# Kernel tuning notes

Measured on AMD Instinct MI355X. Metric: run time of the kernel, lower is better.

The kernel has to match this reference:

```python
import jax, jax.numpy as jnp
import numpy as np

MAX_DEG = 10   # max_degree in DuvenaudMPNN
T = 4          # num_timesteps
NUM_GRAPHS = 64


def setup_inputs() -> dict:
    key = jax.random.key(0)
    ks = jax.random.split(key, 10)
    N, E, IN, EC = 20000, 160000, 64, 16
    s = 0.1
    x = jax.random.normal(ks[0], (N, IN), dtype=jnp.float32)
    edge_index = jax.random.randint(ks[1], (2, E), 0, N)
    edge_attr = jax.random.normal(ks[2], (E, EC), dtype=jnp.float32)
    batch = jnp.sort(jax.random.randint(ks[3], (N,), 0, NUM_GRAPHS))
    # per-timestep, per-degree expert Linear(in+e -> in, bias=False)
    W_msg = jax.random.normal(ks[4], (T, MAX_DEG, IN + EC, IN), dtype=jnp.float32) * s
    # per-timestep readout Linear(in -> 10, bias=False)
    W_read = jax.random.normal(ks[5], (T, IN, 10), dtype=jnp.float32) * s
    fc1_w = jax.random.normal(ks[6], (10, 128), dtype=jnp.float32) * s
    fc1_b = jnp.zeros((128,), jnp.float32)
    fc2_w = jax.random.normal(ks[7], (128, 64), dtype=jnp.float32) * s
    fc2_b = jnp.zeros((64,), jnp.float32)
    fc3_w = jax.random.normal(ks[8], (64, 1), dtype=jnp.float32) * s
    fc3_b = jnp.zeros((1,), jnp.float32)
    return {"x": x, "edge_attr": edge_attr, "W_msg": W_msg, "W_read": W_read,
            "fc1_w": fc1_w, "fc1_b": fc1_b, "fc2_w": fc2_w, "fc2_b": fc2_b,
            "fc3_w": fc3_w, "fc3_b": fc3_b, "edge_index": edge_index, "batch": batch}


def _mpnn(x, edge_attr, W_msg, W_read, edge_index):
    N = x.shape[0]
    # add_self_loops: append (i,i) edges with zero edge features
    self_idx = jnp.arange(N, dtype=edge_index.dtype)
    src = jnp.concatenate([edge_index[0], self_idx])
    dst = jnp.concatenate([edge_index[1], self_idx])
    ea = jnp.concatenate([edge_attr, jnp.zeros((N, edge_attr.shape[1]), edge_attr.dtype)], axis=0)
    # degree of source node (incl. self loop), clamped to MAX_DEG; bucket 0..MAX_DEG-1
    deg = jax.ops.segment_sum(jnp.ones_like(src), src, num_segments=N)
    bucket = jnp.minimum(deg[src], MAX_DEG) - 1
    Etot = src.shape[0]
    for t in range(T):
        mi = jnp.concatenate([x[src], ea], axis=-1)           # [Etot, IN+EC]
        msgs = jnp.zeros((Etot, x.shape[1]), x.dtype)
        for d in range(MAX_DEG):                               # degree-bucketed experts
            md = jax.nn.sigmoid(mi @ W_msg[t, d])              # [Etot, IN]
            msgs = jnp.where((bucket == d)[:, None], md, msgs)
        x = jax.ops.segment_sum(msgs, dst, num_segments=N)    # aggr='add'
    # readout: all timestep heads applied to final x, softmax over outputs, summed
    node_out = jax.nn.softmax(x @ W_read[0], axis=1)
    for t in range(1, T):
        node_out = node_out + jax.nn.softmax(x @ W_read[t], axis=1)
    return node_out                                            # [N, 10]


def reference(x, edge_attr, W_msg, W_read, fc1_w, fc1_b, fc2_w, fc2_b, fc3_w, fc3_b, edge_index, batch):
    node_out = _mpnn(x, edge_attr, W_msg, W_read, edge_index)
    pooled = jax.ops.segment_sum(node_out, batch, num_segments=NUM_GRAPHS)  # global_add_pool
    h = jax.nn.leaky_relu(pooled @ fc1_w + fc1_b)
    h = jax.nn.leaky_relu(h @ fc2_w + fc2_b)
    return jax.nn.leaky_relu(h @ fc3_w + fc3_b)                # [NUM_GRAPHS, 1]
```

## Files before the change

### kernel.cpp

```cpp
#include <hip/hip_runtime.h>

#define MAXD 10
#define TSTEPS 4
#define KD 80
#define IN 64
#define ECH 16
#define TILE_N 64
#define SCAN_CHUNK 1024

#define AGG_BLOCK 256
#define AGG_DPB (AGG_BLOCK / 16)

__device__ __forceinline__ float sigmoidf(float v) {
    return 1.0f / (1.0f + __expf(-v));
}


__global__ __launch_bounds__(256) void hist_kernel(const int* __restrict__ ei,
                                                   int* deg, int* in_cnt, int E) {
    int e = blockIdx.x * 256 + threadIdx.x;
    if (e < E) {
        atomicAdd(&deg[ei[e]], 1);
        atomicAdd(&in_cnt[ei[E + e]], 1);
    }
}


__global__ __launch_bounds__(256) void scanA_kernel(const int* __restrict__ in_cnt,
                                                    const int* __restrict__ deg,
                                                    int* bsum, int* nb_cnt, int N) {
    __shared__ int part[256];
    __shared__ int nbh[MAXD];
    const int t = threadIdx.x;
    if (t < MAXD) nbh[t] = 0;
    __syncthreads();
    const int base = blockIdx.x * SCAN_CHUNK + t * 4;
    int s = 0;
    #pragma unroll
    for (int i = 0; i < 4; ++i) {
        int gi = base + i;
        if (gi < N) {
            s += in_cnt[gi];
            int dg = deg[gi];
            int b = (dg < MAXD - 1) ? dg : (MAXD - 1);
            atomicAdd(&nbh[b], 1);
        }
    }
    part[t] = s;
    __syncthreads();
    for (int off = 128; off > 0; off >>= 1) {
        if (t < off) part[t] += part[t + off];
        __syncthreads();
    }
    if (t == 0) bsum[blockIdx.x] = part[0];
    if (t < MAXD && nbh[t] > 0) atomicAdd(&nb_cnt[t], nbh[t]);
}

__global__ __launch_bounds__(256) void scanB_kernel(int* bsum, int nb,
                                                    const int* __restrict__ nb_cnt,
                                                    int* nb_cursor, int* row_ptr,
                                                    int N, int E) {
    __shared__ int part[256];
    const int t = threadIdx.x;
    int v = (t < nb) ? bsum[t] : 0;
    part[t] = v;
    __syncthreads();
    for (int off = 1; off < 256; off <<= 1) {
        int add = (t >= off) ? part[t - off] : 0;
        __syncthreads();
        part[t] += add;
        __syncthreads();
    }
    if (t < nb) bsum[t] = part[t] - v;
    if (t == 0) {
        int acc = 0;
        for (int b = 0; b < MAXD; ++b) { nb_cursor[b] = acc; acc += nb_cnt[b]; }
        row_ptr[N] = E;
    }
}

__global__ __launch_bounds__(256) void scanC_kernel(const int* __restrict__ in_cnt,
                                                    const int* __restrict__ bsum,
                                                    int* cursorN, int* row_ptr, int N) {
    __shared__ int part[256];
    const int t = threadIdx.x;
    const int base = blockIdx.x * SCAN_CHUNK + t * 4;
    int v[4] = {0, 0, 0, 0};
    #pragma unroll
    for (int i = 0; i < 4; ++i) if (base + i < N) v[i] = in_cnt[base + i];
    const int s = v[0] + v[1] + v[2] + v[3];
    part[t] = s;
    __syncthreads();
    for (int off = 1; off < 256; off <<= 1) {
        int add = (t >= off) ? part[t - off] : 0;
        __syncthreads();
        part[t] += add;
        __syncthreads();
    }
    int a = bsum[blockIdx.x] + part[t] - s;
    #pragma unroll
    for (int i = 0; i < 4; ++i) {
        if (base + i < N) { cursorN[base + i] = a; row_ptr[base + i] = a; }
        a += v[i];
    }
}

__global__ __launch_bounds__(256) void nb_scatter_kernel(const int* __restrict__ deg,
                                                         int* cursor, int* node_list, int N) {
    __shared__ int h[MAXD];
    __shared__ int base[MAXD];
    const int t = threadIdx.x;
    if (t < MAXD) h[t] = 0;
    __syncthreads();
    const int n = blockIdx.x * 256 + t;
    int b = 0, loc = 0;
    const bool valid = n < N;
    if (valid) {
        int dg = deg[n];
        b = (dg < MAXD - 1) ? dg : (MAXD - 1);
        loc = atomicAdd(&h[b], 1);
    }
    __syncthreads();
    if (t < MAXD) base[t] = (h[t] > 0) ? atomicAdd(&cursor[t], h[t]) : 0;
    __syncthreads();
    if (valid) node_list[base[b] + loc] = n;
}

__global__ __launch_bounds__(256) void csr_scatter_kernel(
    const int* __restrict__ ei, const float* __restrict__ ea, const int* __restrict__ deg,
    int* cursor, int* src_csr, int* bkt_csr, float* ea_csr, int E)
{
    int e = blockIdx.x * 256 + threadIdx.x;
    if (e >= E) return;
    int s = ei[e], d = ei[E + e];
    int dg = deg[s];
    int b = (dg < MAXD - 1) ? dg : (MAXD - 1);
    int pos = atomicAdd(&cursor[d], 1);
    src_csr[pos] = s;
    bkt_csr[pos] = b;
    const float4* p = (const float4*)(ea + (size_t)e * ECH);
    float4* o = (float4*)(ea_csr + (size_t)pos * ECH);
    o[0] = p[0]; o[1] = p[1]; o[2] = p[2]; o[3] = p[3];
}


__global__ __launch_bounds__(256) void y_kernel(
    const float* __restrict__ xin, float* __restrict__ y,
    const int* __restrict__ node_list, const int* __restrict__ deg,
    const float* __restrict__ Wt, int N)
{
    __shared__ float Ws[IN][IN];
    __shared__ float Ms[IN][TILE_N + 4];
    __shared__ int id_s[TILE_N];
    __shared__ int bkt_s[TILE_N];

    const int t = threadIdx.x;
    const int i0 = blockIdx.x * TILE_N;
    const int ntile = min(TILE_N, N - i0);

    {
        const int e = t >> 2;
        const bool valid = e < ntile;
        const int c0 = (t & 3) * 16;
        const float4 z4 = make_float4(0.f, 0.f, 0.f, 0.f);
        int node = valid ? node_list[i0 + e] : 0;
        const float* xp = xin + (size_t)node * IN + c0;
        #pragma unroll
        for (int i = 0; i < 16; i += 4) {
            float4 v = valid ? *(const float4*)(xp + i) : z4;
            Ms[c0 + i + 0][e] = v.x; Ms[c0 + i + 1][e] = v.y;
            Ms[c0 + i + 2][e] = v.z; Ms[c0 + i + 3][e] = v.w;
        }
        if (t < TILE_N) {
            if (t < ntile) {
                int id = node_list[i0 + t];
                id_s[t] = id;
                int dg = deg[id];
                bkt_s[t] = (dg < MAXD - 1) ? dg : (MAXD - 1);
            } else { id_s[t] = 0; bkt_s[t] = -1; }
        }
    }
    __syncthreads();

    const int b_first = bkt_s[0];
    const int b_last = bkt_s[ntile - 1];
    const int eg4 = (t >> 4) * 4;
    const int cg4 = (t & 15) * 4;

    for (int b = b_first; b <= b_last; ++b) {
        if (b != b_first) __syncthreads();
        {
            const float4* Wb = (const float4*)(Wt + (size_t)b * KD * IN);
            float4* Wsp = (float4*)Ws;
            #pragma unroll
            for (int q = 0; q < 4; ++q) Wsp[t + q * 256] = Wb[t + q * 256];
        }
        __syncthreads();

        float acc[4][4];
        #pragma unroll
        for (int e2 = 0; e2 < 4; ++e2)
            #pragma unroll
            for (int c = 0; c < 4; ++c) acc[e2][c] = 0.f;

        #pragma unroll 8
        for (int k = 0; k < IN; ++k) {
            const float4 w = *(const float4*)&Ws[k][cg4];
            const float4 m = *(const float4*)&Ms[k][eg4];
            const float me[4] = {m.x, m.y, m.z, m.w};
            #pragma unroll
            for (int e2 = 0; e2 < 4; ++e2) {
                acc[e2][0] += me[e2] * w.x;
                acc[e2][1] += me[e2] * w.y;
                acc[e2][2] += me[e2] * w.z;
                acc[e2][3] += me[e2] * w.w;
            }
        }

        #pragma unroll
        for (int e2 = 0; e2 < 4; ++e2) {
            const int el = eg4 + e2;
            if (el < ntile && bkt_s[el] == b) {
                const size_t o = (size_t)id_s[el] * IN + cg4;
                *(float4*)(y + o) = make_float4(acc[e2][0], acc[e2][1],
                                                acc[e2][2], acc[e2][3]);
            }
        }
    }
}


__global__ __launch_bounds__(AGG_BLOCK) void agg6_kernel(
    const float* __restrict__ y, float* __restrict__ out,
    const int* __restrict__ row_ptr, const int* __restrict__ src_csr,
    const int* __restrict__ bkt_csr, const float* __restrict__ ea_csr,
    const float* __restrict__ Wt, int N)
{
    __shared__ float WeL[MAXD][ECH][IN];
    const int t = threadIdx.x;
    {
        const float4* Wsrc = (const float4*)Wt;
        float4* Wd = (float4*)WeL;
        #pragma unroll
        for (int i = 0; i < MAXD * ECH * IN / 4 / AGG_BLOCK; ++i) {
            int q = t + i * AGG_BLOCK;
            int b = q >> 8;
            int r = q & 255;
            Wd[q] = Wsrc[b * (KD * IN / 4) + (IN * IN / 4) + r];
        }
    }
    __syncthreads();

    const int lane = t & 63;
    const int grp = lane >> 4;
    const int gl = lane & 15;
    const int c0 = gl * 4;
    const int d = blockIdx.x * AGG_DPB + (t >> 6) * 4 + grp;
    if (d >= N) return;
    const int lane0 = grp * 16;

    const int p0 = row_ptr[d];
    const int p1 = row_ptr[d + 1];

    float4 acc = make_float4(0.f, 0.f, 0.f, 0.f);

    for (int p = p0; p < p1; p += 8) {
        const int cnt = min(8, p1 - p);
        const int mi = p + (gl & 7);
        int s_r = 0, b_r = 0;
        if (mi < p1) { s_r = src_csr[mi]; b_r = bkt_csr[mi]; }

        float4 yv[8];
        #pragma unroll
        for (int i = 0; i < 8; ++i) {
            int si = __shfl(s_r, lane0 + i);
            if (i < cnt) yv[i] = *(const float4*)(y + (size_t)si * IN + c0);
        }

        const float4* eab = (const float4*)(ea_csr + (size_t)p * ECH);
        float4 ca0 = eab[0], ca1 = eab[1], ca2 = eab[2], ca3 = eab[3];

        #pragma unroll
        for (int i = 0; i < 8; ++i) {
            if (i < cnt) {
                float4 na0, na1, na2, na3;
                if (i + 1 < cnt) {
                    const float4* ep = (const float4*)(ea_csr + (size_t)(p + i + 1) * ECH);
                    na0 = ep[0]; na1 = ep[1]; na2 = ep[2]; na3 = ep[3];
                } else {
                    na0 = na1 = na2 = na3 = make_float4(0.f, 0.f, 0.f, 0.f);
                }
                const int b = __shfl(b_r, lane0 + i);
                const float ev[16] = {ca0.x, ca0.y, ca0.z, ca0.w, ca1.x, ca1.y, ca1.z, ca1.w,
                                      ca2.x, ca2.y, ca2.z, ca2.w, ca3.x, ca3.y, ca3.z, ca3.w};
                float4 z = make_float4(0.f, 0.f, 0.f, 0.f);
                #pragma unroll
                for (int k = 0; k < ECH; ++k) {
                    const float4 w = *(const float4*)&WeL[b][k][c0];
                    z.x += ev[k] * w.x; z.y += ev[k] * w.y;
                    z.z += ev[k] * w.z; z.w += ev[k] * w.w;
                }
                acc.x += sigmoidf(yv[i].x + z.x);
                acc.y += sigmoidf(yv[i].y + z.y);
                acc.z += sigmoidf(yv[i].z + z.z);
                acc.w += sigmoidf(yv[i].w + z.w);
                ca0 = na0; ca1 = na1; ca2 = na2; ca3 = na3;
            }
        }
    }

    const float4 yd = *(const float4*)(y + (size_t)d * IN + c0);
    float4 r = make_float4(sigmoidf(yd.x) + acc.x, sigmoidf(yd.y) + acc.y,
                           sigmoidf(yd.z) + acc.z, sigmoidf(yd.w) + acc.w);
    *(float4*)(out + (size_t)d * IN + c0) = r;
}


__global__ __launch_bounds__(256) void readout_kernel(
    const float* __restrict__ x, const float* __restrict__ Wr,
    const int* __restrict__ batch, float* __restrict__ pooled, int N)
{
    __shared__ float Wr_s[TSTEPS][10][IN];
    __shared__ float pool_s[64 * 10];
    const int t = threadIdx.x;
    for (int idx = t; idx < TSTEPS * IN * 10; idx += 256) {
        int tt = idx / (IN * 10);
        int r = idx % (IN * 10);
        int k = r / 10;
        int j = r % 10;
        Wr_s[tt][j][k] = Wr[idx];
    }
    for (int idx = t; idx < 64 * 10; idx += 256) pool_s[idx] = 0.f;
    __syncthreads();

    const int n = blockIdx.x * 256 + t;
    if (n < N) {
        float xr[IN];
        const float4* xp = (const float4*)(x + (size_t)n * IN);
        #pragma unroll
        for (int i = 0; i < IN / 4; ++i) ((float4*)xr)[i] = xp[i];
        float out10[10];
        #pragma unroll
        for (int j = 0; j < 10; ++j) out10[j] = 0.f;
        for (int tt = 0; tt < TSTEPS; ++tt) {
            float lg[10];
            #pragma unroll
            for (int j = 0; j < 10; ++j) {
                const float4* wp = (const float4*)Wr_s[tt][j];
                float s = 0.f;
                #pragma unroll
                for (int i = 0; i < IN / 4; ++i) {
                    float4 w = wp[i];
                    float4 xv = ((const float4*)xr)[i];
                    s += w.x * xv.x + w.y * xv.y + w.z * xv.z + w.w * xv.w;
                }
                lg[j] = s;
            }
            float mx = lg[0];
            #pragma unroll
            for (int j = 1; j < 10; ++j) mx = fmaxf(mx, lg[j]);
            float sum = 0.f;
            #pragma unroll
            for (int j = 0; j < 10; ++j) { lg[j] = __expf(lg[j] - mx); sum += lg[j]; }
            float inv = 1.f / sum;
            #pragma unroll
            for (int j = 0; j < 10; ++j) out10[j] += lg[j] * inv;
        }
        const int g = batch[n];
        #pragma unroll
        for (int j = 0; j < 10; ++j) atomicAdd(&pool_s[g * 10 + j], out10[j]);
    }
    __syncthreads();
    for (int idx = t; idx < 64 * 10; idx += 256) {
        float v = pool_s[idx];
        if (v != 0.f) atomicAdd(&pooled[idx], v);
    }
}


__global__ __launch_bounds__(256) void mlp_kernel(
    const float* __restrict__ pooled,
    const float* __restrict__ fc1w, const float* __restrict__ fc1b,
    const float* __restrict__ fc2w, const float* __restrict__ fc2b,
    const float* __restrict__ fc3w, const float* __restrict__ fc3b,
    float* __restrict__ out, int G)
{
    __shared__ float p_s[64 * 10];
    __shared__ float h1[64 * 128];
    __shared__ float h2[64 * 64];
    const int t = threadIdx.x;
    for (int idx = t; idx < G * 10; idx += 256) p_s[idx] = pooled[idx];
    __syncthreads();
    for (int idx = t; idx < G * 128; idx += 256) {
        int g = idx >> 7, j = idx & 127;
        float s = fc1b[j];
        #pragma unroll
        for (int k = 0; k < 10; ++k) s += p_s[g * 10 + k] * fc1w[k * 128 + j];
        h1[idx] = (s > 0.f) ? s : 0.01f * s;
    }
    __syncthreads();
    for (int idx = t; idx < G * 64; idx += 256) {
        int g = idx >> 6, j = idx & 63;
        float s = fc2b[j];
        for (int k = 0; k < 128; ++k) s += h1[(g << 7) + k] * fc2w[(k << 6) + j];
        h2[idx] = (s > 0.f) ? s : 0.01f * s;
    }
    __syncthreads();
    if (t < G) {
        float s = fc3b[0];
        for (int k = 0; k < 64; ++k) s += h2[(t << 6) + k] * fc3w[k];
        out[t] = (s > 0.f) ? s : 0.01f * s;
    }
}


extern "C" void kernel_launch(void* const* d_in, const int* in_sizes, int n_in,
                              void* d_out, int out_size, void* d_ws, size_t ws_size,
                              hipStream_t stream)
{
    const float* x     = (const float*)d_in[0];
    const float* ea    = (const float*)d_in[1];
    const float* Wmsg  = (const float*)d_in[2];
    const float* Wread = (const float*)d_in[3];
    const float* fc1w  = (const float*)d_in[4];
    const float* fc1b  = (const float*)d_in[5];
    const float* fc2w  = (const float*)d_in[6];
    const float* fc2b  = (const float*)d_in[7];
    const float* fc3w  = (const float*)d_in[8];
    const float* fc3b  = (const float*)d_in[9];
    const int* ei      = (const int*)d_in[10];
    const int* batch   = (const int*)d_in[11];

    const int N = in_sizes[0] / IN;
    const int E = in_sizes[10] / 2;
    const int nscan = (N + SCAN_CHUNK - 1) / SCAN_CHUNK;

    char* ws = (char*)d_ws;
    size_t off = 0;
    auto take = [&](size_t bytes) {
        char* p = ws + off;
        off = (off + bytes + 255) & ~(size_t)255;
        return p;
    };
    int* meta      = (int*)take(128);
    float* pooled  = (float*)take(64 * 10 * 4);
    int* deg       = (int*)take((size_t)N * 4);
    int* in_cnt    = (int*)take((size_t)N * 4);
    const size_t zero_bytes = (size_t)((char*)in_cnt - (char*)meta) + (size_t)N * 4;
    int* bsum      = (int*)take((size_t)nscan * 4);
    int* node_list = (int*)take((size_t)N * 4);
    int* cursorN   = (int*)take((size_t)N * 4);
    int* row_ptr   = (int*)take((size_t)(N + 1) * 4);
    int* src_csr   = (int*)take((size_t)E * 4);
    int* bkt_csr   = (int*)take((size_t)E * 4);
    float* ea_csr  = (float*)take((size_t)E * ECH * 4);
    float* ybuf    = (float*)take((size_t)N * IN * 4);
    float* xbA     = (float*)take((size_t)N * IN * 4);
    float* xbB     = (float*)take((size_t)N * IN * 4);

    int* nb_cnt    = meta;
    int* nb_cursor = meta + 16;

    const int nbN = (N + 255) / 256;
    const int nbE = (E + 255) / 256;

    hipMemsetAsync(meta, 0, zero_bytes, stream);
    hist_kernel<<<nbE, 256, 0, stream>>>(ei, deg, in_cnt, E);
    scanA_kernel<<<nscan, 256, 0, stream>>>(in_cnt, deg, bsum, nb_cnt, N);
    scanB_kernel<<<1, 256, 0, stream>>>(bsum, nscan, nb_cnt, nb_cursor, row_ptr, N, E);
    scanC_kernel<<<nscan, 256, 0, stream>>>(in_cnt, bsum, cursorN, row_ptr, N);
    nb_scatter_kernel<<<nbN, 256, 0, stream>>>(deg, nb_cursor, node_list, N);
    csr_scatter_kernel<<<nbE, 256, 0, stream>>>(ei, ea, deg, cursorN,
                                                src_csr, bkt_csr, ea_csr, E);

    const int nblkY = (N + TILE_N - 1) / TILE_N;
    const int nblkA = (N + AGG_DPB - 1) / AGG_DPB;
    const float* xi = x;
    float* bufs[2] = {xbA, xbB};
    for (int tt = 0; tt < TSTEPS; ++tt) {
        const float* Wt = Wmsg + (size_t)tt * MAXD * KD * IN;
        float* xo = bufs[tt & 1];
        y_kernel<<<nblkY, 256, 0, stream>>>(xi, ybuf, node_list, deg, Wt, N);
        agg6_kernel<<<nblkA, AGG_BLOCK, 0, stream>>>(ybuf, xo, row_ptr, src_csr,
                                                     bkt_csr, ea_csr, Wt, N);
        xi = xo;
    }

    readout_kernel<<<nbN, 256, 0, stream>>>(xi, Wread, batch, pooled, N);
    mlp_kernel<<<1, 256, 0, stream>>>(pooled, fc1w, fc1b, fc2w, fc2b, fc3w, fc3b,
                                      (float*)d_out, out_size);
}
```

Baseline: 310.7 us.

## Precompute edge-feature message terms for all timesteps in bucket-sorted batched GEMM

Edges are now also scattered into degree-bucket order, and one batched kernel computes the edge-attribute projection ea·W_e for every timestep up front into a [T,E,64] buffer. The per-timestep aggregation kernel then only gathers the precomputed z rows through a CSR-to-bucket index instead of doing a 16-deep per-edge matvec from shared-memory weights. This removes the per-edge FMA work and the 40KB shared-memory weight load from the aggregation kernel. In exchange it writes and reads about 164MB of extra z data, so the gather becomes more memory-bound.

New measurement: 304.2 us. -2.1%, faster.

```diff
diff --git a/kernel.cpp b/kernel.cpp
--- a/kernel.cpp
+++ b/kernel.cpp
@@ -6,6 +6,7 @@
 #define IN 64
 #define ECH 16
 #define TILE_N 64
+#define TILE_Z 128
 #define SCAN_CHUNK 1024
 
 #define AGG_BLOCK 256
@@ -25,14 +26,15 @@
     }
 }
 
-
 __global__ __launch_bounds__(256) void scanA_kernel(const int* __restrict__ in_cnt,
                                                     const int* __restrict__ deg,
-                                                    int* bsum, int* nb_cnt, int N) {
+                                                    int* bsum, int* nb_cnt, int* eb_cnt,
+                                                    int N) {
     __shared__ int part[256];
     __shared__ int nbh[MAXD];
-    const int t = threadIdx.x;
-    if (t < MAXD) nbh[t] = 0;
+    __shared__ int ebh[MAXD];
+    const int t = threadIdx.x;
+    if (t < MAXD) { nbh[t] = 0; ebh[t] = 0; }
     __syncthreads();
     const int base = blockIdx.x * SCAN_CHUNK + t * 4;
     int s = 0;
@@ -44,6 +46,7 @@
             int dg = deg[gi];
             int b = (dg < MAXD - 1) ? dg : (MAXD - 1);
             atomicAdd(&nbh[b], 1);
+            if (dg > 0) atomicAdd(&ebh[b], dg);
         }
     }
     part[t] = s;
@@ -53,13 +56,18 @@
         __syncthreads();
     }
     if (t == 0) bsum[blockIdx.x] = part[0];
-    if (t < MAXD && nbh[t] > 0) atomicAdd(&nb_cnt[t], nbh[t]);
+    if (t < MAXD) {
+        if (nbh[t] > 0) atomicAdd(&nb_cnt[t], nbh[t]);
+        if (ebh[t] > 0) atomicAdd(&eb_cnt[t], ebh[t]);
+    }
 }
 
 __global__ __launch_bounds__(256) void scanB_kernel(int* bsum, int nb,
                                                     const int* __restrict__ nb_cnt,
-                                                    int* nb_cursor, int* row_ptr,
-                                                    int N, int E) {
+                                                    int* nb_cursor,
+                                                    const int* __restrict__ eb_cnt,
+                                                    int* eb_cursor, int* eb_base,
+                                                    int* row_ptr, int N, int E) {
     __shared__ int part[256];
     const int t = threadIdx.x;
     int v = (t < nb) ? bsum[t] : 0;
@@ -75,6 +83,11 @@
     if (t == 0) {
         int acc = 0;
         for (int b = 0; b < MAXD; ++b) { nb_cursor[b] = acc; acc += nb_cnt[b]; }
+        acc = 0;
+        for (int b = 0; b < MAXD; ++b) {
+            eb_cursor[b] = acc; eb_base[b] = acc; acc += eb_cnt[b];
+        }
+        eb_base[MAXD] = E;
         row_ptr[N] = E;
     }
 }
@@ -126,21 +139,119 @@
     if (valid) node_list[base[b] + loc] = n;
 }
 
-__global__ __launch_bounds__(256) void csr_scatter_kernel(
+__global__ __launch_bounds__(256) void edge_scatter_kernel(
     const int* __restrict__ ei, const float* __restrict__ ea, const int* __restrict__ deg,
-    int* cursor, int* src_csr, int* bkt_csr, float* ea_csr, int E)
-{
-    int e = blockIdx.x * 256 + threadIdx.x;
-    if (e >= E) return;
-    int s = ei[e], d = ei[E + e];
-    int dg = deg[s];
-    int b = (dg < MAXD - 1) ? dg : (MAXD - 1);
-    int pos = atomicAdd(&cursor[d], 1);
-    src_csr[pos] = s;
-    bkt_csr[pos] = b;
-    const float4* p = (const float4*)(ea + (size_t)e * ECH);
-    float4* o = (float4*)(ea_csr + (size_t)pos * ECH);
-    o[0] = p[0]; o[1] = p[1]; o[2] = p[2]; o[3] = p[3];
+    int* cursorN, int* eb_cursor,
+    int* src_csr, int* csr2bkt, float* ea_bkt, int E)
+{
+    __shared__ int h[MAXD];
+    __shared__ int hbase[MAXD];
+    const int t = threadIdx.x;
+    if (t < MAXD) h[t] = 0;
+    __syncthreads();
+    const int e = blockIdx.x * 256 + t;
+    const bool valid = e < E;
+    int s = 0, d = 0, b = 0, loc = 0;
+    if (valid) {
+        s = ei[e]; d = ei[E + e];
+        int dg = deg[s];
+        b = (dg < MAXD - 1) ? dg : (MAXD - 1);
+        loc = atomicAdd(&h[b], 1);
+    }
+    __syncthreads();
+    if (t < MAXD) hbase[t] = (h[t] > 0) ? atomicAdd(&eb_cursor[t], h[t]) : 0;
+    __syncthreads();
+    if (valid) {
+        const int posz = hbase[b] + loc;
+        const int pos = atomicAdd(&cursorN[d], 1);
+        src_csr[pos] = s;
+        csr2bkt[pos] = posz;
+        const float4* p = (const float4*)(ea + (size_t)e * ECH);
+        float4* o = (float4*)(ea_bkt + (size_t)posz * ECH);
+        o[0] = p[0]; o[1] = p[1]; o[2] = p[2]; o[3] = p[3];
+    }
+}
+
+
+__global__ __launch_bounds__(256) void zgemm_kernel(
+    const float* __restrict__ ea_bkt, float* __restrict__ zs,
+    const int* __restrict__ eb_base, const float* __restrict__ Wmsg,
+    int E, int ntiles)
+{
+    __shared__ float Ez[ECH][TILE_Z + 4];
+    __shared__ int ebase_s[MAXD + 1];
+
+    const int t = threadIdx.x;
+    const int bid = blockIdx.x;
+    const int tt = bid / ntiles;
+    const int i0 = (bid % ntiles) * TILE_Z;
+    const float* Wt = Wmsg + (size_t)tt * MAXD * KD * IN;
+    float* zt = zs + (size_t)tt * E * IN;
+    const int ntile = min(TILE_Z, E - i0);
+
+    if (t <= MAXD) ebase_s[t] = eb_base[t];
+    {
+        const int e = t >> 1;
+        const int j0 = (t & 1) * 8;
+        const bool valid = e < ntile;
+        const float4 z4 = make_float4(0.f, 0.f, 0.f, 0.f);
+        const float* ep = ea_bkt + (size_t)(i0 + e) * ECH + j0;
+        #pragma unroll
+        for (int i = 0; i < 8; i += 4) {
+            float4 v = valid ? *(const float4*)(ep + i) : z4;
+            Ez[j0 + i + 0][e] = v.x; Ez[j0 + i + 1][e] = v.y;
+            Ez[j0 + i + 2][e] = v.z; Ez[j0 + i + 3][e] = v.w;
+        }
+    }
+    __syncthreads();
+
+    const int eg8 = (t >> 4) * 8;
+    const int cg4 = (t & 15) * 4;
+
+    int b = 0;
+    #pragma unroll
+    for (int q = 1; q < MAXD; ++q) if (ebase_s[q] <= i0) b = q;
+
+    for (; b < MAXD; ++b) {
+        const int slo = max(ebase_s[b] - i0, 0);
+        const int shi = min(ebase_s[b + 1] - i0, ntile);
+        if (shi > slo) {
+            const float* wp = Wt + ((size_t)b * KD + IN) * IN + cg4;
+            float4 w[ECH];
+            #pragma unroll
+            for (int k = 0; k < ECH; ++k) w[k] = *(const float4*)(wp + (size_t)k * IN);
+
+            float acc[8][4];
+            #pragma unroll
+            for (int e2 = 0; e2 < 8; ++e2)
+                #pragma unroll
+                for (int c = 0; c < 4; ++c) acc[e2][c] = 0.f;
+
+            #pragma unroll
+            for (int k = 0; k < ECH; ++k) {
+                const float4 m0 = *(const float4*)&Ez[k][eg8];
+                const float4 m1 = *(const float4*)&Ez[k][eg8 + 4];
+                const float me[8] = {m0.x, m0.y, m0.z, m0.w, m1.x, m1.y, m1.z, m1.w};
+                #pragma unroll
+                for (int e2 = 0; e2 < 8; ++e2) {
+                    acc[e2][0] += me[e2] * w[k].x;
+                    acc[e2][1] += me[e2] * w[k].y;
+                    acc[e2][2] += me[e2] * w[k].z;
+                    acc[e2][3] += me[e2] * w[k].w;
+                }
+            }
+
+            #pragma unroll
+            for (int e2 = 0; e2 < 8; ++e2) {
+                const int el = eg8 + e2;
+                if (el >= slo && el < shi) {
+                    *(float4*)(zt + (size_t)(i0 + el) * IN + cg4) =
+                        make_float4(acc[e2][0], acc[e2][1], acc[e2][2], acc[e2][3]);
+                }
+            }
+        }
+        if (ebase_s[b + 1] >= i0 + ntile) break;
+    }
 }
 
 
@@ -230,27 +341,12 @@
 }
 
 
-__global__ __launch_bounds__(AGG_BLOCK) void agg6_kernel(
+__global__ __launch_bounds__(AGG_BLOCK) void aggS_kernel(
     const float* __restrict__ y, float* __restrict__ out,
     const int* __restrict__ row_ptr, const int* __restrict__ src_csr,
-    const int* __restrict__ bkt_csr, const float* __restrict__ ea_csr,
-    const float* __restrict__ Wt, int N)
-{
-    __shared__ float WeL[MAXD][ECH][IN];
-    const int t = threadIdx.x;
-    {
-        const float4* Wsrc = (const float4*)Wt;
-        float4* Wd = (float4*)WeL;
-        #pragma unroll
-        for (int i = 0; i < MAXD * ECH * IN / 4 / AGG_BLOCK; ++i) {
-            int q = t + i * AGG_BLOCK;
-            int b = q >> 8;
-            int r = q & 255;
-            Wd[q] = Wsrc[b * (KD * IN / 4) + (IN * IN / 4) + r];
-        }
-    }
-    __syncthreads();
-
+    const int* __restrict__ csr2bkt, const float* __restrict__ zt, int N)
+{
+    const int t = threadIdx.x;
     const int lane = t & 63;
     const int grp = lane >> 4;
     const int gl = lane & 15;
@@ -267,44 +363,26 @@
     for (int p = p0; p < p1; p += 8) {
         const int cnt = min(8, p1 - p);
         const int mi = p + (gl & 7);
-        int s_r = 0, b_r = 0;
-        if (mi < p1) { s_r = src_csr[mi]; b_r = bkt_csr[mi]; }
-
-        float4 yv[8];
+        int s_r = 0, z_r = 0;
+        if (mi < p1) { s_r = src_csr[mi]; z_r = csr2bkt[mi]; }
+
+        float4 yv[8], zv[8];
         #pragma unroll
         for (int i = 0; i < 8; ++i) {
             int si = __shfl(s_r, lane0 + i);
-            if (i < cnt) yv[i] = *(const float4*)(y + (size_t)si * IN + c0);
-        }
-
-        const float4* eab = (const float4*)(ea_csr + (size_t)p * ECH);
-        float4 ca0 = eab[0], ca1 = eab[1], ca2 = eab[2], ca3 = eab[3];
-
+            int zi = __shfl(z_r, lane0 + i);
+            if (i < cnt) {
+                yv[i] = *(const float4*)(y + (size_t)si * IN + c0);
+                zv[i] = *(const float4*)(zt + (size_t)zi * IN + c0);
+            }
+        }
         #pragma unroll
         for (int i = 0; i < 8; ++i) {
             if (i < cnt) {
-                float4 na0, na1, na2, na3;
-                if (i + 1 < cnt) {
-                    const float4* ep = (const float4*)(ea_csr + (size_t)(p + i + 1) * ECH);
-                    na0 = ep[0]; na1 = ep[1]; na2 = ep[2]; na3 = ep[3];
-                } else {
-                    na0 = na1 = na2 = na3 = make_float4(0.f, 0.f, 0.f, 0.f);
-                }
-                const int b = __shfl(b_r, lane0 + i);
-                const float ev[16] = {ca0.x, ca0.y, ca0.z, ca0.w, ca1.x, ca1.y, ca1.z, ca1.w,
-                                      ca2.x, ca2.y, ca2.z, ca2.w, ca3.x, ca3.y, ca3.z, ca3.w};
-                float4 z = make_float4(0.f, 0.f, 0.f, 0.f);
-                #pragma unroll
-                for (int k = 0; k < ECH; ++k) {
-                    const float4 w = *(const float4*)&WeL[b][k][c0];
-                    z.x += ev[k] * w.x; z.y += ev[k] * w.y;
-                    z.z += ev[k] * w.z; z.w += ev[k] * w.w;
-                }
-                acc.x += sigmoidf(yv[i].x + z.x);
-                acc.y += sigmoidf(yv[i].y + z.y);
-                acc.z += sigmoidf(yv[i].z + z.z);
-                acc.w += sigmoidf(yv[i].w + z.w);
-                ca0 = na0; ca1 = na1; ca2 = na2; ca3 = na3;
+                acc.x += sigmoidf(yv[i].x + zv[i].x);
+                acc.y += sigmoidf(yv[i].y + zv[i].y);
+                acc.z += sigmoidf(yv[i].z + zv[i].z);
+                acc.w += sigmoidf(yv[i].w + zv[i].w);
             }
         }
     }
@@ -434,6 +512,7 @@
     const int N = in_sizes[0] / IN;
     const int E = in_sizes[10] / 2;
     const int nscan = (N + SCAN_CHUNK - 1) / SCAN_CHUNK;
+    const int ntilesZ = (E + TILE_Z - 1) / TILE_Z;
 
     char* ws = (char*)d_ws;
     size_t off = 0;
@@ -442,7 +521,7 @@
         off = (off + bytes + 255) & ~(size_t)255;
         return p;
     };
-    int* meta      = (int*)take(128);
+    int* meta      = (int*)take(512);
     float* pooled  = (float*)take(64 * 10 * 4);
     int* deg       = (int*)take((size_t)N * 4);
     int* in_cnt    = (int*)take((size_t)N * 4);
@@ -452,26 +531,33 @@
     int* cursorN   = (int*)take((size_t)N * 4);
     int* row_ptr   = (int*)take((size_t)(N + 1) * 4);
     int* src_csr   = (int*)take((size_t)E * 4);
-    int* bkt_csr   = (int*)take((size_t)E * 4);
-    float* ea_csr  = (float*)take((size_t)E * ECH * 4);
+    int* csr2bkt   = (int*)take((size_t)E * 4);
+    float* ea_bkt  = (float*)take((size_t)E * ECH * 4);
+    float* zs      = (float*)take((size_t)TSTEPS * E * IN * 4);
     float* ybuf    = (float*)take((size_t)N * IN * 4);
     float* xbA     = (float*)take((size_t)N * IN * 4);
     float* xbB     = (float*)take((size_t)N * IN * 4);
 
     int* nb_cnt    = meta;
     int* nb_cursor = meta + 16;
+    int* eb_cnt    = meta + 32;
+    int* eb_cursor = meta + 48;
+    int* eb_base   = meta + 64;
 
     const int nbN = (N + 255) / 256;
     const int nbE = (E + 255) / 256;
 
     hipMemsetAsync(meta, 0, zero_bytes, stream);
     hist_kernel<<<nbE, 256, 0, stream>>>(ei, deg, in_cnt, E);
-    scanA_kernel<<<nscan, 256, 0, stream>>>(in_cnt, deg, bsum, nb_cnt, N);
-    scanB_kernel<<<1, 256, 0, stream>>>(bsum, nscan, nb_cnt, nb_cursor, row_ptr, N, E);
+    scanA_kernel<<<nscan, 256, 0, stream>>>(in_cnt, deg, bsum, nb_cnt, eb_cnt, N);
+    scanB_kernel<<<1, 256, 0, stream>>>(bsum, nscan, nb_cnt, nb_cursor,
+                                        eb_cnt, eb_cursor, eb_base, row_ptr, N, E);
     scanC_kernel<<<nscan, 256, 0, stream>>>(in_cnt, bsum, cursorN, row_ptr, N);
     nb_scatter_kernel<<<nbN, 256, 0, stream>>>(deg, nb_cursor, node_list, N);
-    csr_scatter_kernel<<<nbE, 256, 0, stream>>>(ei, ea, deg, cursorN,
-                                                src_csr, bkt_csr, ea_csr, E);
+    edge_scatter_kernel<<<nbE, 256, 0, stream>>>(ei, ea, deg, cursorN, eb_cursor,
+                                                 src_csr, csr2bkt, ea_bkt, E);
+    zgemm_kernel<<<TSTEPS * ntilesZ, 256, 0, stream>>>(ea_bkt, zs, eb_base, Wmsg,
+                                                       E, ntilesZ);
 
     const int nblkY = (N + TILE_N - 1) / TILE_N;
     const int nblkA = (N + AGG_DPB - 1) / AGG_DPB;
@@ -481,8 +567,9 @@
         const float* Wt = Wmsg + (size_t)tt * MAXD * KD * IN;
         float* xo = bufs[tt & 1];
         y_kernel<<<nblkY, 256, 0, stream>>>(xi, ybuf, node_list, deg, Wt, N);
-        agg6_kernel<<<nblkA, AGG_BLOCK, 0, stream>>>(ybuf, xo, row_ptr, src_csr,
-                                                     bkt_csr, ea_csr, Wt, N);
+        aggS_kernel<<<nblkA, AGG_BLOCK, 0, stream>>>(ybuf, xo, row_ptr, src_csr,
+                                                     csr2bkt,
+                                                     zs + (size_t)tt * E * IN, N);
         xi = xo;
     }
 
```
